# Optimization experiments

Measured on AMD Instinct MI355X. Metric: run time of the kernel, lower is better.

## Reference

```python
import jax, jax.numpy as jnp
import numpy as np

NUM_HEADS = 16
DIM = 1024

def setup_inputs() -> dict:
    key = jax.random.key(0)
    ks = jax.random.split(key, 12)
    B, N, T, C = 4, 4096, 77, DIM
    s = 1.0 / np.sqrt(C)
    return {
        "hidden_states": jax.random.normal(ks[0], (B, N, C), jnp.float32),
        "encoder_hidden_states": jax.random.normal(ks[1], (B, T, C), jnp.float32),
        "attention_mask": jnp.zeros((B, N, T), jnp.float32),
        "Wq": jax.random.normal(ks[2], (C, C), jnp.float32) * s,
        "bq": jnp.zeros((C,), jnp.float32),
        "Wk": jax.random.normal(ks[3], (C, C), jnp.float32) * s,
        "bk": jnp.zeros((C,), jnp.float32),
        "Wv": jax.random.normal(ks[4], (C, C), jnp.float32) * s,
        "bv": jnp.zeros((C,), jnp.float32),
        "Wo": jax.random.normal(ks[5], (C, C), jnp.float32) * s,
        "bo": jnp.zeros((C,), jnp.float32),
    }

def reference(hidden_states, encoder_hidden_states, attention_mask,
              Wq, bq, Wk, bk, Wv, bv, Wo, bo):
    B, N, C = hidden_states.shape
    T = encoder_hidden_states.shape[1]
    H = NUM_HEADS
    D = C // H
    # QKV projections (torch Linear: x @ W.T + b)
    q = (hidden_states @ Wq.T + bq).reshape(B, N, H, D).transpose(0, 2, 1, 3)   # bhnd
    k = (encoder_hidden_states @ Wk.T + bk).reshape(B, T, H, D).transpose(0, 2, 1, 3)  # bhtd
    v = (encoder_hidden_states @ Wv.T + bv).reshape(B, T, H, D).transpose(0, 2, 1, 3)  # bhtd
    scale = 1.0 / jnp.sqrt(jnp.asarray(D, q.dtype))
    # scores [B,H,N,T]; additive mask broadcast over heads
    scores = jnp.einsum('bhnd,bhtd->bhnt', q, k) * scale + attention_mask[:, None, :, :]
    attn = jax.nn.softmax(scores, axis=-1)
    out = jnp.einsum('bhnt,bhtd->bhnd', attn, v)
    out = out.transpose(0, 2, 1, 3).reshape(B, N, C)
    return out @ Wo.T + bo
```

## Files before the change

### kernel.cpp

```cpp
#include <hip/hip_runtime.h>
#include <cstdint>

typedef __bf16 bf16x8 __attribute__((ext_vector_type(8)));
typedef float f32x4 __attribute__((ext_vector_type(4)));
typedef unsigned short u16;
typedef unsigned int u32;

__device__ __forceinline__ u16 f2bf(float f) {
    u32 u = __builtin_bit_cast(u32, f);
    u += 0x7fffu + ((u >> 16) & 1u);
    return (u16)(u >> 16);
}

__device__ __forceinline__ void gl_lds16(const u16* g, u16* l) {
    __builtin_amdgcn_global_load_lds(
        (const __attribute__((address_space(1))) void*)g,
        (__attribute__((address_space(3))) void*)l,
        16, 0, 0);
}

__device__ __forceinline__ f32x4 mfma16(bf16x8 a, bf16x8 b, f32x4 c) {
    return __builtin_amdgcn_mfma_f32_16x16x32_bf16(a, b, c, 0, 0, 0);
}

__global__ void cvt_pad(const float* __restrict__ src, u16* __restrict__ dst,
                        int srcn, int totn) {
    int i = (blockIdx.x * 256 + threadIdx.x) * 4;
    if (i >= totn) return;
    float4 v = make_float4(0.f, 0.f, 0.f, 0.f);
    if (i < srcn) v = *(const float4*)&src[i];
    ushort4 o;
    o.x = f2bf(v.x); o.y = f2bf(v.y); o.z = f2bf(v.z); o.w = f2bf(v.w);
    *(ushort4*)&dst[i] = o;
}

struct CvtArgs {
    const float* s[5];
    u16* d[5];
    int srcn[5];
    int totn[5];
};

__global__ void cvt_multi(CvtArgs a) {
    const int seg = blockIdx.y;
    int i = (blockIdx.x * 256 + threadIdx.x) * 4;
    if (i >= a.totn[seg]) return;
    float4 v = make_float4(0.f, 0.f, 0.f, 0.f);
    if (i < a.srcn[seg]) v = *(const float4*)&a.s[seg][i];
    ushort4 o;
    o.x = f2bf(v.x); o.y = f2bf(v.y); o.z = f2bf(v.z); o.w = f2bf(v.w);
    *(ushort4*)&a.d[seg][i] = o;
}

__device__ __forceinline__ void store_out(u16* C, long idx, float v) { C[idx] = f2bf(v); }
__device__ __forceinline__ void store_out(float* C, long idx, float v) { C[idx] = v; }

template <typename OutT>
__global__ __launch_bounds__(512, 2) void gemm8p(
    const u16* __restrict__ A, const u16* __restrict__ W,
    const float* __restrict__ bias, OutT* __restrict__ C,
    int M, int N, int K) {
    __shared__ __align__(16) u16 As[4][256 * 32];
    __shared__ __align__(16) u16 Bs[4][256 * 32];

    const int tid = threadIdx.x;
    const int wid = tid >> 6, l = tid & 63;
    const int wr = wid >> 2, wc = wid & 3;
    const int l15 = l & 15, lg = l >> 4;

    const int lin = blockIdx.y * gridDim.x + blockIdx.x;
    const int cpx = (gridDim.x * gridDim.y) >> 3;
    const int swz = (lin & 7) * cpx + (lin >> 3);
    const long tn = swz % gridDim.x;
    const long tm = swz / gridDim.x;

    const u16* Ab = A + tm * 256 * (long)K;
    const u16* Bb = W + tn * 256 * (long)K;

    const int srow = tid >> 2;
    const int sch = (tid & 3) ^ (srow & 3) ^ ((srow >> 2) & 3);
    const long asrc = (long)srow * K + sch * 8;

    const int rch = (lg ^ (l15 & 3) ^ ((l15 >> 2) & 3)) * 8;

    const int NT = K >> 5;

#define STAGE_A(ss, t_)                                                       \
    do {                                                                      \
        u16* p_ = &As[ss][0];                                                 \
        gl_lds16(Ab + asrc + (long)(t_)*32, p_ + tid * 8);                    \
        gl_lds16(Ab + 128L * K + asrc + (long)(t_)*32, p_ + 4096 + tid * 8);  \
    } while (0)
#define STAGE_B(ss, t_)                                                       \
    do {                                                                      \
        u16* p_ = &Bs[ss][0];                                                 \
        gl_lds16(Bb + asrc + (long)(t_)*32, p_ + tid * 8);                    \
        gl_lds16(Bb + 128L * K + asrc + (long)(t_)*32, p_ + 4096 + tid * 8);  \
    } while (0)

    f32x4 acc[8][4] = {};

    STAGE_A(0, 0); STAGE_B(0, 0);
    STAGE_A(1, 1); STAGE_B(1, 1);
    asm volatile("s_waitcnt vmcnt(4)" ::: "memory");
    __builtin_amdgcn_sched_barrier(0);
    __builtin_amdgcn_s_barrier();

    for (int t0 = 0; t0 < NT; t0 += 4) {
#pragma unroll
        for (int u = 0; u < 4; ++u) {
            const int t = t0 + u;
            const int slot = u;
            const int ss = (u + 2) & 3;
            const bool st = (t + 2) < NT;

            bf16x8 a[4], b[4];
#pragma unroll
            for (int mf = 0; mf < 4; ++mf)
                a[mf] = *(const bf16x8*)&As[slot][(wr * 128 + mf * 16 + l15) * 32 + rch];
#pragma unroll
            for (int nf = 0; nf < 4; ++nf)
                b[nf] = *(const bf16x8*)&Bs[slot][(wc * 64 + nf * 16 + l15) * 32 + rch];
            if (st) STAGE_A(ss, t + 2);
            __builtin_amdgcn_s_barrier();
            asm volatile("s_waitcnt lgkmcnt(0)" ::: "memory");
            __builtin_amdgcn_sched_barrier(0);
            __builtin_amdgcn_s_setprio(1);
#pragma unroll
            for (int mf = 0; mf < 4; ++mf)
#pragma unroll
                for (int nf = 0; nf < 4; ++nf)
                    acc[mf][nf] = mfma16(a[mf], b[nf], acc[mf][nf]);
            __builtin_amdgcn_s_setprio(0);
            __builtin_amdgcn_s_barrier();

            bf16x8 a2[4];
#pragma unroll
            for (int mf = 0; mf < 4; ++mf)
                a2[mf] = *(const bf16x8*)&As[slot][(wr * 128 + (mf + 4) * 16 + l15) * 32 + rch];
            if (st) STAGE_B(ss, t + 2);
            __builtin_amdgcn_s_barrier();
            asm volatile("s_waitcnt lgkmcnt(0)" ::: "memory");
            __builtin_amdgcn_sched_barrier(0);
            __builtin_amdgcn_s_setprio(1);
#pragma unroll
            for (int mf = 0; mf < 4; ++mf)
#pragma unroll
                for (int nf = 0; nf < 4; ++nf)
                    acc[mf + 4][nf] = mfma16(a2[mf], b[nf], acc[mf + 4][nf]);
            __builtin_amdgcn_s_setprio(0);
            if (st)
                asm volatile("s_waitcnt vmcnt(4)" ::: "memory");
            else
                asm volatile("s_waitcnt vmcnt(0)" ::: "memory");
            __builtin_amdgcn_sched_barrier(0);
            __builtin_amdgcn_s_barrier();
        }
    }
#undef STAGE_A
#undef STAGE_B

    const long row0 = tm * 256 + wr * 128;
    const long col0 = tn * 256 + wc * 64;
    float bv[4];
#pragma unroll
    for (int nf = 0; nf < 4; ++nf) bv[nf] = bias[col0 + nf * 16 + l15];
#pragma unroll
    for (int mf = 0; mf < 8; ++mf)
#pragma unroll
        for (int nf = 0; nf < 4; ++nf)
#pragma unroll
            for (int r = 0; r < 4; ++r) {
                const long row = row0 + mf * 16 + lg * 4 + r;
                const long col = col0 + nf * 16 + l15;
                store_out(C, row * N + col, acc[mf][nf][r] + bv[nf]);
            }
}

__device__ __forceinline__ void gemm128_body(
    const u16* __restrict__ A, const u16* __restrict__ W,
    const float* __restrict__ bias, u16* __restrict__ C,
    int N, int K) {
    __shared__ u16 As[128 * 64];
    __shared__ u16 Bs[128 * 64];
    const int tid = threadIdx.x;
    const int w = tid >> 6, l = tid & 63;
    const int wr = w >> 1, wc = w & 1;
    const int l15 = l & 15, lg = l >> 4;
    const long tm = blockIdx.y, tn = blockIdx.x;
    const u16* Ab = A + tm * 128 * (long)K;
    const u16* Bb = W + tn * 128 * (long)K;

    f32x4 acc[4][4] = {};

    for (int k0 = 0; k0 < K; k0 += 64) {
#pragma unroll
        for (int t = 0; t < 4; ++t) {
            int i = t * 256 + tid;
            int row = i >> 3, cc = i & 7;
            gl_lds16(Ab + (long)row * K + k0 + cc * 8, &As[i * 8]);
            gl_lds16(Bb + (long)row * K + k0 + cc * 8, &Bs[i * 8]);
        }
        __syncthreads();
#pragma unroll
        for (int kk = 0; kk < 64; kk += 32) {
            bf16x8 a[4], b[4];
#pragma unroll
            for (int m = 0; m < 4; ++m)
                a[m] = *(const bf16x8*)&As[(wr * 64 + m * 16 + l15) * 64 + kk + lg * 8];
#pragma unroll
            for (int n = 0; n < 4; ++n)
                b[n] = *(const bf16x8*)&Bs[(wc * 64 + n * 16 + l15) * 64 + kk + lg * 8];
#pragma unroll
            for (int m = 0; m < 4; ++m)
#pragma unroll
                for (int n = 0; n < 4; ++n)
                    acc[m][n] = mfma16(a[m], b[n], acc[m][n]);
        }
        __syncthreads();
    }

    const long row0 = tm * 128 + wr * 64;
    const long col0 = tn * 128 + wc * 64;
#pragma unroll
    for (int m = 0; m < 4; ++m)
#pragma unroll
        for (int n = 0; n < 4; ++n)
#pragma unroll
            for (int r = 0; r < 4; ++r) {
                const long row = row0 + m * 16 + lg * 4 + r;
                const long col = col0 + n * 16 + l15;
                C[row * N + col] = f2bf(acc[m][n][r] + bias[col]);
            }
}

__global__ __launch_bounds__(256) void gemm_kv(
    const u16* __restrict__ A,
    const u16* __restrict__ Wk, const float* __restrict__ bk, u16* __restrict__ Ko,
    const u16* __restrict__ Wv, const float* __restrict__ bv, u16* __restrict__ Vo,
    int N, int K) {
    const bool isv = blockIdx.z != 0;
    gemm128_body(A, isv ? Wv : Wk, isv ? bv : bk, isv ? Vo : Ko, N, K);
}

__global__ __launch_bounds__(256) void attn_fused(
    const u16* __restrict__ Q,
    const u16* __restrict__ Kb,
    const u16* __restrict__ Vb,
    const float* __restrict__ mask,
    u16* __restrict__ Ao) {
    __shared__ u16 Ks[96 * 64];
    __shared__ u16 Vt[64 * 96];
    __shared__ u16 Ps[128 * 96];

    const int b = blockIdx.z, h = blockIdx.y, nt = blockIdx.x;
    const int tid = threadIdx.x;
    const int w = tid >> 6, l = tid & 63;
    const int l15 = l & 15, lg = l >> 4;

    for (int c = tid; c < 768; c += 256) {
        const int t = c >> 3, dc = c & 7;
        union { uint4 u; u16 s[8]; } kv, vv;
        kv.u = make_uint4(0, 0, 0, 0);
        vv.u = make_uint4(0, 0, 0, 0);
        if (t < 77) {
            const long base = ((long)(b * 77 + t)) * 1024 + h * 64 + dc * 8;
            kv.u = *(const uint4*)&Kb[base];
            vv.u = *(const uint4*)&Vb[base];
        }
        *(uint4*)&Ks[t * 64 + dc * 8] = kv.u;
#pragma unroll
        for (int j = 0; j < 8; ++j) Vt[(dc * 8 + j) * 96 + t] = vv.s[j];
    }
    __syncthreads();

    f32x4 acc[2][6] = {};
    const long qrow0 = (long)b * 4096 + nt * 128 + w * 32;
#pragma unroll
    for (int kk = 0; kk < 64; kk += 32) {
        bf16x8 a[2], kf[6];
#pragma unroll
        for (int m = 0; m < 2; ++m)
            a[m] = *(const bf16x8*)&Q[(qrow0 + m * 16 + l15) * 1024 + h * 64 + kk + lg * 8];
#pragma unroll
        for (int n = 0; n < 6; ++n)
            kf[n] = *(const bf16x8*)&Ks[(n * 16 + l15) * 64 + kk + lg * 8];
#pragma unroll
        for (int m = 0; m < 2; ++m)
#pragma unroll
            for (int n = 0; n < 6; ++n)
                acc[m][n] = mfma16(a[m], kf[n], acc[m][n]);
    }

    const float* mbase = mask + ((long)b * 4096 + nt * 128 + w * 32) * 77;
#pragma unroll
    for (int m = 0; m < 2; ++m) {
#pragma unroll
        for (int r = 0; r < 4; ++r) {
            const int row = m * 16 + lg * 4 + r;
            float vals[6];
            float rmax = -3e38f;
#pragma unroll
            for (int n = 0; n < 6; ++n) {
                const int col = n * 16 + l15;
                float v = -3e38f;
                if (col < 77) v = acc[m][n][r] * 0.125f + mbase[row * 77 + col];
                vals[n] = v;
                rmax = fmaxf(rmax, v);
            }
#pragma unroll
            for (int off = 1; off < 16; off <<= 1)
                rmax = fmaxf(rmax, __shfl_xor(rmax, off, 64));
            float s = 0.f;
#pragma unroll
            for (int n = 0; n < 6; ++n) {
                float e = (vals[n] > -1e37f) ? __expf(vals[n] - rmax) : 0.f;
                vals[n] = e;
                s += e;
            }
#pragma unroll
            for (int off = 1; off < 16; off <<= 1)
                s += __shfl_xor(s, off, 64);
            const float inv = 1.f / s;
#pragma unroll
            for (int n = 0; n < 6; ++n)
                Ps[(w * 32 + row) * 96 + n * 16 + l15] = f2bf(vals[n] * inv);
        }
    }
    __syncthreads();

    f32x4 o[2][4] = {};
#pragma unroll
    for (int kt = 0; kt < 96; kt += 32) {
        bf16x8 a[2], vf[4];
#pragma unroll
        for (int m = 0; m < 2; ++m)
            a[m] = *(const bf16x8*)&Ps[(w * 32 + m * 16 + l15) * 96 + kt + lg * 8];
#pragma unroll
        for (int n = 0; n < 4; ++n)
            vf[n] = *(const bf16x8*)&Vt[(n * 16 + l15) * 96 + kt + lg * 8];
#pragma unroll
        for (int m = 0; m < 2; ++m)
#pragma unroll
            for (int n = 0; n < 4; ++n)
                o[m][n] = mfma16(a[m], vf[n], o[m][n]);
    }

#pragma unroll
    for (int m = 0; m < 2; ++m)
#pragma unroll
        for (int n = 0; n < 4; ++n)
#pragma unroll
            for (int r = 0; r < 4; ++r) {
                const long row = (long)b * 4096 + nt * 128 + w * 32 + m * 16 + lg * 4 + r;
                const int col = h * 64 + n * 16 + l15;
                Ao[row * 1024 + col] = f2bf(o[m][n][r]);
            }
}

extern "C" void kernel_launch(void* const* d_in, const int* in_sizes, int n_in,
                              void* d_out, int out_size, void* d_ws, size_t ws_size,
                              hipStream_t stream) {
    const float* hidden = (const float*)d_in[0];
    const float* enc = (const float*)d_in[1];
    const float* mask = (const float*)d_in[2];
    const float* Wq = (const float*)d_in[3];
    const float* bq = (const float*)d_in[4];
    const float* Wk = (const float*)d_in[5];
    const float* bk = (const float*)d_in[6];
    const float* Wv = (const float*)d_in[7];
    const float* bv = (const float*)d_in[8];
    const float* Wo = (const float*)d_in[9];
    const float* bo = (const float*)d_in[10];
    float* out = (float*)d_out;

    char* ws = (char*)d_ws;
    u16* hiddenB = (u16*)(ws);
    u16* Qb = (u16*)(ws + 33554432L);
    u16* AoB = (u16*)(ws + 2 * 33554432L);
    u16* WqB = (u16*)(ws + 3 * 33554432L);
    u16* WkB = WqB + 1048576;
    u16* WvB = WkB + 1048576;
    u16* WoB = WvB + 1048576;
    u16* encB = WoB + 1048576;
    u16* Kbuf = encB + 393216;
    u16* Vbuf = Kbuf + 393216;

    cvt_pad<<<dim3(16384), 256, 0, stream>>>(hidden, hiddenB, 16777216, 16777216);
    CvtArgs ca;
    ca.s[0] = Wq;  ca.d[0] = WqB; ca.srcn[0] = 1048576; ca.totn[0] = 1048576;
    ca.s[1] = Wk;  ca.d[1] = WkB; ca.srcn[1] = 1048576; ca.totn[1] = 1048576;
    ca.s[2] = Wv;  ca.d[2] = WvB; ca.srcn[2] = 1048576; ca.totn[2] = 1048576;
    ca.s[3] = Wo;  ca.d[3] = WoB; ca.srcn[3] = 1048576; ca.totn[3] = 1048576;
    ca.s[4] = enc; ca.d[4] = encB; ca.srcn[4] = 315392; ca.totn[4] = 393216;
    cvt_multi<<<dim3(1024, 5), 256, 0, stream>>>(ca);

    gemm8p<u16><<<dim3(4, 64), 512, 0, stream>>>(hiddenB, WqB, bq, Qb, 16384, 1024, 1024);
    gemm_kv<<<dim3(8, 3, 2), 256, 0, stream>>>(encB, WkB, bk, Kbuf, WvB, bv, Vbuf, 1024, 1024);

    attn_fused<<<dim3(32, 16, 4), 256, 0, stream>>>(Qb, Kbuf, Vbuf, mask, AoB);

    gemm8p<float><<<dim3(4, 64), 512, 0, stream>>>(AoB, WoB, bo, out, 16384, 1024, 1024);
}
```

Before: 171.8 us.

## Switch GEMM to BK=64 double-buffered LDS with four-phase staged prefetch

The bf16 GEMM kernel moves from four 32-wide K stages to two 64-wide K buffers, with an 8-way XOR swizzle on LDS chunks. Each K step is split into four MFMA phases, and the prefetch loads for the next tiles are spread across those phases. This halves the number of outer iterations and should amortize barriers and waitcnts over more MFMA work per stage. In exchange, the prefetch schedule and vmcnt accounting become more intricate, which risks hazards if the load ordering is wrong. LDS use stays the same.

```diff
diff --git a/kernel.cpp b/kernel.cpp
--- a/kernel.cpp
+++ b/kernel.cpp
@@ -60,8 +60,8 @@
     const u16* __restrict__ A, const u16* __restrict__ W,
     const float* __restrict__ bias, OutT* __restrict__ C,
     int M, int N, int K) {
-    __shared__ __align__(16) u16 As[4][256 * 32];
-    __shared__ __align__(16) u16 Bs[4][256 * 32];
+    __shared__ __align__(16) u16 As[2][256 * 64];
+    __shared__ __align__(16) u16 Bs[2][256 * 64];
 
     const int tid = threadIdx.x;
     const int wid = tid >> 6, l = tid & 63;
@@ -77,80 +77,139 @@
     const u16* Ab = A + tm * 256 * (long)K;
     const u16* Bb = W + tn * 256 * (long)K;
 
-    const int srow = tid >> 2;
-    const int sch = (tid & 3) ^ (srow & 3) ^ ((srow >> 2) & 3);
-    const long asrc = (long)srow * K + sch * 8;
-
-    const int rch = (lg ^ (l15 & 3) ^ ((l15 >> 2) & 3)) * 8;
-
-    const int NT = K >> 5;
-
-#define STAGE_A(ss, t_)                                                       \
-    do {                                                                      \
-        u16* p_ = &As[ss][0];                                                 \
-        gl_lds16(Ab + asrc + (long)(t_)*32, p_ + tid * 8);                    \
-        gl_lds16(Ab + 128L * K + asrc + (long)(t_)*32, p_ + 4096 + tid * 8);  \
-    } while (0)
-#define STAGE_B(ss, t_)                                                       \
-    do {                                                                      \
-        u16* p_ = &Bs[ss][0];                                                 \
-        gl_lds16(Bb + asrc + (long)(t_)*32, p_ + tid * 8);                    \
-        gl_lds16(Bb + 128L * K + asrc + (long)(t_)*32, p_ + 4096 + tid * 8);  \
-    } while (0)
+    const int srow = tid >> 3;
+    const int schunk = (tid & 7) ^ (srow & 7);
+    const long srcoff = (long)srow * K + schunk * 8;
+
+    const int rxor = l15 & 7;
+    const int rdo0 = ((0 * 4 + lg) ^ rxor) * 8;
+    const int rdo1 = ((1 * 4 + lg) ^ rxor) * 8;
+
+    const int NT = K >> 6;
+
+#define STAGE_A(bufi, q_, t_)                                                 \
+    gl_lds16(Ab + (long)(q_)*64 * K + srcoff + (long)(t_)*64,                 \
+             &As[bufi][(q_)*4096 + tid * 8])
+#define STAGE_B(bufi, q_, t_)                                                 \
+    gl_lds16(Bb + (long)(q_)*64 * K + srcoff + (long)(t_)*64,                 \
+             &Bs[bufi][(q_)*4096 + tid * 8])
 
     f32x4 acc[8][4] = {};
 
-    STAGE_A(0, 0); STAGE_B(0, 0);
-    STAGE_A(1, 1); STAGE_B(1, 1);
-    asm volatile("s_waitcnt vmcnt(4)" ::: "memory");
+#pragma unroll
+    for (int q = 0; q < 4; ++q) { STAGE_A(0, q, 0); STAGE_B(0, q, 0); }
+#pragma unroll
+    for (int q = 0; q < 4; ++q) STAGE_B(1, q, 1);
+    STAGE_A(1, 0, 1); STAGE_A(1, 2, 1);
+    asm volatile("s_waitcnt vmcnt(6)" ::: "memory");
     __builtin_amdgcn_sched_barrier(0);
     __builtin_amdgcn_s_barrier();
 
-    for (int t0 = 0; t0 < NT; t0 += 4) {
-#pragma unroll
-        for (int u = 0; u < 4; ++u) {
-            const int t = t0 + u;
-            const int slot = u;
-            const int ss = (u + 2) & 3;
-            const bool st = (t + 2) < NT;
-
-            bf16x8 a[4], b[4];
-#pragma unroll
-            for (int mf = 0; mf < 4; ++mf)
-                a[mf] = *(const bf16x8*)&As[slot][(wr * 128 + mf * 16 + l15) * 32 + rch];
-#pragma unroll
-            for (int nf = 0; nf < 4; ++nf)
-                b[nf] = *(const bf16x8*)&Bs[slot][(wc * 64 + nf * 16 + l15) * 32 + rch];
-            if (st) STAGE_A(ss, t + 2);
+    const int arow = wr * 128 + l15;
+    const int brow = wc * 64 + l15;
+
+    for (int t = 0; t < NT; ++t) {
+        const int c = t & 1;
+        const u16* __restrict__ Ap = &As[c][0];
+        const u16* __restrict__ Bp = &Bs[c][0];
+        const bool s1 = (t + 1) < NT;
+        const bool s2 = (t + 2) < NT;
+        bf16x8 b[4][2];
+
+        {
+            bf16x8 a[2][2];
+#pragma unroll
+            for (int mi = 0; mi < 2; ++mi) {
+                a[mi][0] = *(const bf16x8*)&Ap[(arow + mi * 16) * 64 + rdo0];
+                a[mi][1] = *(const bf16x8*)&Ap[(arow + mi * 16) * 64 + rdo1];
+            }
+#pragma unroll
+            for (int nf = 0; nf < 4; ++nf) {
+                b[nf][0] = *(const bf16x8*)&Bp[(brow + nf * 16) * 64 + rdo0];
+                b[nf][1] = *(const bf16x8*)&Bp[(brow + nf * 16) * 64 + rdo1];
+            }
+            if (s1) STAGE_A(c ^ 1, 1, t + 1);
             __builtin_amdgcn_s_barrier();
             asm volatile("s_waitcnt lgkmcnt(0)" ::: "memory");
             __builtin_amdgcn_sched_barrier(0);
             __builtin_amdgcn_s_setprio(1);
 #pragma unroll
-            for (int mf = 0; mf < 4; ++mf)
-#pragma unroll
-                for (int nf = 0; nf < 4; ++nf)
-                    acc[mf][nf] = mfma16(a[mf], b[nf], acc[mf][nf]);
+            for (int mi = 0; mi < 2; ++mi)
+#pragma unroll
+                for (int nf = 0; nf < 4; ++nf) {
+                    acc[mi][nf] = mfma16(a[mi][0], b[nf][0], acc[mi][nf]);
+                    acc[mi][nf] = mfma16(a[mi][1], b[nf][1], acc[mi][nf]);
+                }
             __builtin_amdgcn_s_setprio(0);
             __builtin_amdgcn_s_barrier();
-
-            bf16x8 a2[4];
-#pragma unroll
-            for (int mf = 0; mf < 4; ++mf)
-                a2[mf] = *(const bf16x8*)&As[slot][(wr * 128 + (mf + 4) * 16 + l15) * 32 + rch];
-            if (st) STAGE_B(ss, t + 2);
+        }
+        {
+            bf16x8 a[2][2];
+#pragma unroll
+            for (int mi = 0; mi < 2; ++mi) {
+                a[mi][0] = *(const bf16x8*)&Ap[(arow + (mi + 2) * 16) * 64 + rdo0];
+                a[mi][1] = *(const bf16x8*)&Ap[(arow + (mi + 2) * 16) * 64 + rdo1];
+            }
+            if (s1) STAGE_A(c ^ 1, 3, t + 1);
+            if (s2) { STAGE_B(c, 0, t + 2); STAGE_B(c, 1, t + 2); }
             __builtin_amdgcn_s_barrier();
             asm volatile("s_waitcnt lgkmcnt(0)" ::: "memory");
             __builtin_amdgcn_sched_barrier(0);
             __builtin_amdgcn_s_setprio(1);
 #pragma unroll
-            for (int mf = 0; mf < 4; ++mf)
-#pragma unroll
-                for (int nf = 0; nf < 4; ++nf)
-                    acc[mf + 4][nf] = mfma16(a2[mf], b[nf], acc[mf + 4][nf]);
+            for (int mi = 0; mi < 2; ++mi)
+#pragma unroll
+                for (int nf = 0; nf < 4; ++nf) {
+                    acc[mi + 2][nf] = mfma16(a[mi][0], b[nf][0], acc[mi + 2][nf]);
+                    acc[mi + 2][nf] = mfma16(a[mi][1], b[nf][1], acc[mi + 2][nf]);
+                }
             __builtin_amdgcn_s_setprio(0);
-            if (st)
-                asm volatile("s_waitcnt vmcnt(4)" ::: "memory");
+            __builtin_amdgcn_s_barrier();
+        }
+        {
+            bf16x8 a[2][2];
+#pragma unroll
+            for (int mi = 0; mi < 2; ++mi) {
+                a[mi][0] = *(const bf16x8*)&Ap[(arow + (mi + 4) * 16) * 64 + rdo0];
+                a[mi][1] = *(const bf16x8*)&Ap[(arow + (mi + 4) * 16) * 64 + rdo1];
+            }
+            if (s2) { STAGE_B(c, 2, t + 2); STAGE_B(c, 3, t + 2); STAGE_A(c, 0, t + 2); }
+            __builtin_amdgcn_s_barrier();
+            asm volatile("s_waitcnt lgkmcnt(0)" ::: "memory");
+            __builtin_amdgcn_sched_barrier(0);
+            __builtin_amdgcn_s_setprio(1);
+#pragma unroll
+            for (int mi = 0; mi < 2; ++mi)
+#pragma unroll
+                for (int nf = 0; nf < 4; ++nf) {
+                    acc[mi + 4][nf] = mfma16(a[mi][0], b[nf][0], acc[mi + 4][nf]);
+                    acc[mi + 4][nf] = mfma16(a[mi][1], b[nf][1], acc[mi + 4][nf]);
+                }
+            __builtin_amdgcn_s_setprio(0);
+            __builtin_amdgcn_s_barrier();
+        }
+        {
+            bf16x8 a[2][2];
+#pragma unroll
+            for (int mi = 0; mi < 2; ++mi) {
+                a[mi][0] = *(const bf16x8*)&Ap[(arow + (mi + 6) * 16) * 64 + rdo0];
+                a[mi][1] = *(const bf16x8*)&Ap[(arow + (mi + 6) * 16) * 64 + rdo1];
+            }
+            if (s2) STAGE_A(c, 2, t + 2);
+            __builtin_amdgcn_s_barrier();
+            asm volatile("s_waitcnt lgkmcnt(0)" ::: "memory");
+            __builtin_amdgcn_sched_barrier(0);
+            __builtin_amdgcn_s_setprio(1);
+#pragma unroll
+            for (int mi = 0; mi < 2; ++mi)
+#pragma unroll
+                for (int nf = 0; nf < 4; ++nf) {
+                    acc[mi + 6][nf] = mfma16(a[mi][0], b[nf][0], acc[mi + 6][nf]);
+                    acc[mi + 6][nf] = mfma16(a[mi][1], b[nf][1], acc[mi + 6][nf]);
+                }
+            __builtin_amdgcn_s_setprio(0);
+            if (s2)
+                asm volatile("s_waitcnt vmcnt(6)" ::: "memory");
             else
                 asm volatile("s_waitcnt vmcnt(0)" ::: "memory");
             __builtin_amdgcn_sched_barrier(0);
```

After: 163.3 us. -5.0%, faster.
